# Optimization experiments

Hardware: AMD Instinct MI355X
Metric: run time of the kernel (lower is better)

The kernel has to match this reference:

```python
import jax, jax.numpy as jnp
import numpy as np

B, T, U, C, N, K = 128, 800, 64, 80, 512, 10


def setup_inputs() -> dict:
    key = jax.random.key(0)
    ks = jax.random.split(key, 8)
    s = 0.05
    return {
        "x": jax.random.normal(ks[0], (B, T, 3), jnp.float32),
        "sentence_inputs": jax.random.uniform(ks[1], (B, U, C), jnp.float32),
        "sentence_lengths": jax.random.randint(ks[2], (B,), 1, U + 1, jnp.int32),
        "W_x": jax.random.normal(ks[3], (3 + C, 4 * N), jnp.float32) * s,
        "W_h": jax.random.normal(ks[4], (N, 4 * N), jnp.float32) * s,
        "b": jnp.zeros((4 * N,), jnp.float32),
        "W_win": jax.random.normal(ks[5], (N, 3 * K), jnp.float32) * s,
        "b_win": jnp.zeros((3 * K,), jnp.float32),
    }


def reference(x, sentence_inputs, sentence_lengths, W_x, W_h, b, W_win, b_win):
    # mask over character positions: [B, 1, U]
    u = jnp.arange(1, U + 1, dtype=jnp.float32)                 # 1..U as in tf.range
    mask = (jnp.arange(U)[None, :] < sentence_lengths[:, None]).astype(jnp.float32)

    def step(carry, x_t):
        h, c, kappa, w = carry
        xi = jnp.concatenate([x_t, w], axis=-1)                 # [B, 3+C]
        z = xi @ W_x + h @ W_h + b                              # [B, 4N]
        zi, zf, zg, zo = jnp.split(z, 4, axis=-1)               # keras gate order i,f,c,o
        i = jax.nn.sigmoid(zi)
        f = jax.nn.sigmoid(zf)
        g = jnp.tanh(zg)
        o = jax.nn.sigmoid(zo)
        c = f * c + i * g
        h = o * jnp.tanh(c)
        win = h @ W_win + b_win                                 # [B, 3K]
        a_hat, b_hat, k_hat = jnp.split(win, 3, axis=-1)
        alpha = jnp.exp(a_hat)[:, :, None]                      # [B, K, 1]
        beta = jnp.exp(b_hat)[:, :, None]
        kappa = kappa + jnp.exp(k_hat)                          # [B, K]
        # Gaussian window weights phi: [B, U]
        phi = jnp.sum(alpha * jnp.exp(-beta * (kappa[:, :, None] - u) ** 2), axis=1)
        phi = phi * mask
        w = jnp.einsum('bu,buc->bc', phi, sentence_inputs)      # [B, C]
        return (h, c, kappa, w), (h, phi, w)

    h0 = jnp.zeros((B, N), jnp.float32)
    c0 = jnp.zeros((B, N), jnp.float32)
    k0 = jnp.zeros((B, K), jnp.float32)
    w0 = jnp.zeros((B, C), jnp.float32)
    _, (h_seq, phi_seq, w_seq) = jax.lax.scan(
        step, (h0, c0, k0, w0), jnp.swapaxes(x, 0, 1))
    # time-major -> batch-major
    return (jnp.swapaxes(h_seq, 0, 1),
            jnp.swapaxes(phi_seq, 0, 1),
            jnp.swapaxes(w_seq, 0, 1))
```

## Files before the change

### kernel.cpp

```cpp
#include <hip/hip_runtime.h>
#include <hip/hip_bf16.h>

#define Tt   800
#define Uu   64
#define Cc   80
#define NBLK 128
#define ASTR 648
#define ALIMB 10368

#define HB_G    32768
#define HB_BUF  16384
#define HB_LIMB 8192

#define OUT_PHI 52428800u
#define OUT_W   58982400u

#define WS_HBUF  0u
#define WS_SEQ   524288u
#define WS_SENTT 524800u
#define WS_NEED  3146240u
#define POLL_CAP 2000000

typedef __attribute__((ext_vector_type(4))) int   i32x4;
typedef __attribute__((ext_vector_type(8))) short short8;
typedef __attribute__((ext_vector_type(4))) float f32x4;
typedef unsigned long long u64;

__device__ __forceinline__ float b2f(unsigned short u){ unsigned int i = ((unsigned int)u)<<16; float f; __builtin_memcpy(&f,&i,4); return f; }
__device__ __forceinline__ unsigned short f2b(float f){ __hip_bfloat16 h = __float2bfloat16(f); unsigned short u; __builtin_memcpy(&u,&h,2); return u; }
__device__ __forceinline__ float sigm(float v){ return 1.f/(1.f + __expf(-v)); }
__device__ __forceinline__ float tanh_(float v){ return 1.f - 2.f/(1.f + __expf(2.f*v)); }

__device__ __forceinline__ void drain_vm(){ asm volatile("s_waitcnt vmcnt(0)" ::: "memory"); }
#define WAIT_VM(N) asm volatile("s_waitcnt vmcnt(" #N ")" ::: "memory")

__device__ __forceinline__ void gld16(i32x4* dst, const void* addr) {
  asm volatile("global_load_dwordx4 %0, %1, off sc0 sc1" : "=v"(*dst) : "v"(addr));
}
__device__ __forceinline__ void gst16(void* addr, i32x4 v) {
  asm volatile("global_store_dwordx4 %0, %1, off sc0 sc1" :: "v"(addr), "v"(v) : "memory");
}
__device__ __forceinline__ int gld4(const int* p) {
  int v;
  asm volatile("global_load_dword %0, %1, off sc0 sc1" : "=v"(v) : "v"(p));
  asm volatile("s_waitcnt vmcnt(0)" ::: "memory");
  return v;
}
__device__ __forceinline__ void gst4(int* p, int v) {
  asm volatile("global_store_dword %0, %1, off sc0 sc1" :: "v"(p), "v"(v) : "memory");
}

__global__ void prep(const float* __restrict__ sent,
                     unsigned short* __restrict__ hbuf, int* __restrict__ seq,
                     float* __restrict__ sentT) {
  int i = blockIdx.x*256 + threadIdx.x;
  if (i < 262144) hbuf[i] = 0;
  else if (i < 262272) seq[i - 262144] = 0;
  int j = i - 262272;
  if (j >= 0 && j < 655360) {
    int r = j / 5120, rem = j % 5120, c = rem >> 6, u = rem & 63;
    sentT[j] = sent[r*5120 + u*80 + c];
  }
}

__global__ __launch_bounds__(512, 1) void rnn_main(
    const float* __restrict__ x,
    const int*   __restrict__ slen,
    const float* __restrict__ bias,
    const float* __restrict__ bwin,
    const float* __restrict__ Wwin,
    const float* __restrict__ Wx,
    const float* __restrict__ Wh,
    unsigned short* __restrict__ hbuf,
    int* __restrict__ seq,
    const float* __restrict__ sentT,
    float* __restrict__ out)
{
  __shared__ __align__(16) unsigned short lA[2*ALIMB];
  __shared__ __align__(16) unsigned short lWwF[32768];
  __shared__ __align__(16) float lPart[8*2*64*4];
  __shared__ float lWin[16*32];
  __shared__ float lE[16*32];
  __shared__ float lKap[16*16];
  __shared__ float lPhi[16*64];
  __shared__ __align__(16) unsigned short lHout[2*16*32];
  __shared__ float lBwin[32];
  __shared__ int   lLen[16];

  const int g    = blockIdx.x >> 4;
  const int jj   = blockIdx.x & 15;
  const int grow = g*16 + jj;
  const int tid  = threadIdx.x;
  const int wave = tid >> 6;
  const int lane = tid & 63;
  const int l15  = lane & 15, lhi = lane >> 4;

  int* seqG = seq + g*16;
  unsigned short* hbG = hbuf + g*HB_G;

  for (int i = tid; i < 2*ALIMB/4; i += 512) ((u64*)lA)[i] = 0;
  for (int e = tid; e < 16384; e += 512) {
    int j = e & 7, ln = (e >> 3) & 63, nt = (e >> 9) & 1, kt = e >> 10;
    int k   = kt*32 + (ln >> 4)*8 + j;
    int col = nt*16 + (ln & 15);
    float v = (col < 30) ? Wwin[k*30 + col] : 0.f;
    unsigned short hi = f2b(v);
    lWwF[e]         = hi;
    lWwF[16384 + e] = f2b(v - b2f(hi));
  }
  if (tid < 32)  lBwin[tid] = (tid < 30) ? bwin[tid] : 0.f;
  if (tid < 16)  lLen[tid]  = slen[g*16 + tid];
  for (int i = tid; i < 256; i += 512) lKap[i] = 0.f;

  short8 bfh[20], bfl[20];
  const int zc = (l15 >> 2)*512 + jj*32 + wave*4 + (l15 & 3);
  #pragma unroll
  for (int kt = 0; kt < 20; ++kt) {
    short8 hv, lv;
    #pragma unroll
    for (int j = 0; j < 8; ++j) {
      int k = kt*32 + lhi*8 + j;
      float v;
      if (k < 512)      v = Wh[(size_t)k*2048 + zc];
      else if (k < 515) v = Wx[(size_t)(k-512)*2048 + zc];
      else if (k < 544) v = 0.f;
      else if (k < 624) v = Wx[(size_t)(3 + (k-544))*2048 + zc];
      else              v = 0.f;
      unsigned short hh = f2b(v);
      hv[j] = (short)hh;
      lv[j] = (short)f2b(v - b2f(hh));
    }
    bfh[kt] = hv;
    bfl[kt] = lv;
  }
  const float bias_r = bias[zc];
  __syncthreads();

  float c_reg[4] = {0.f,0.f,0.f,0.f};

  auto phaseW = [&](int tt, bool writeState) {
    {
      f32x4 aw0 = {0.f,0.f,0.f,0.f}, aw1 = {0.f,0.f,0.f,0.f};
      #pragma unroll
      for (int kk = 0; kk < 2; ++kk) {
        const int kt = wave*2 + kk;
        short8 ah = *(const short8*)&lA[l15*ASTR + kt*32 + lhi*8];
        short8 al = *(const short8*)&lA[ALIMB + l15*ASTR + kt*32 + lhi*8];
        short8 bh0 = *(const short8*)&lWwF[((kt*2+0)*64 + lane)*8];
        short8 bl0 = *(const short8*)&lWwF[16384 + ((kt*2+0)*64 + lane)*8];
        short8 bh1 = *(const short8*)&lWwF[((kt*2+1)*64 + lane)*8];
        short8 bl1 = *(const short8*)&lWwF[16384 + ((kt*2+1)*64 + lane)*8];
        aw0 = __builtin_amdgcn_mfma_f32_16x16x32_bf16(ah, bh0, aw0, 0,0,0);
        aw0 = __builtin_amdgcn_mfma_f32_16x16x32_bf16(ah, bl0, aw0, 0,0,0);
        aw0 = __builtin_amdgcn_mfma_f32_16x16x32_bf16(al, bh0, aw0, 0,0,0);
        aw1 = __builtin_amdgcn_mfma_f32_16x16x32_bf16(ah, bh1, aw1, 0,0,0);
        aw1 = __builtin_amdgcn_mfma_f32_16x16x32_bf16(ah, bl1, aw1, 0,0,0);
        aw1 = __builtin_amdgcn_mfma_f32_16x16x32_bf16(al, bh1, aw1, 0,0,0);
      }
      *(f32x4*)&lPart[((wave*2+0)*64 + lane)*4] = aw0;
      *(f32x4*)&lPart[((wave*2+1)*64 + lane)*4] = aw1;
    }
    __syncthreads();
    {
      const int nt = tid >> 8, row = (tid >> 4) & 15, col = tid & 15;
      const int ln = ((row >> 2) << 4) | col, reg = row & 3;
      float s = 0.f;
      #pragma unroll
      for (int w = 0; w < 8; ++w) s += lPart[((w*2 + nt)*64 + ln)*4 + reg];
      lWin[row*32 + nt*16 + col] = s + lBwin[nt*16 + col];
    }
    __syncthreads();
    {
      const int r = tid >> 5, j = tid & 31;
      if (j < 30) lE[r*32 + j] = __expf(lWin[r*32 + j]);
    }
    __syncthreads();
    if (tid < 160) {
      const int r = tid / 10, k = tid % 10;
      lKap[r*16 + k] += lE[r*32 + 20 + k];
    }
    __syncthreads();
    #pragma unroll
    for (int it2 = 0; it2 < 2; ++it2) {
      const int pair = tid + it2*512;
      const int r = pair >> 6, u = pair & 63;
      const float u1 = (float)u + 1.f;
      float phi = 0.f;
      #pragma unroll
      for (int k = 0; k < 10; ++k) {
        float d = lKap[r*16 + k] - u1;
        phi += lE[r*32 + k] * __expf(-lE[r*32 + 10 + k] * d * d);
      }
      if (u >= lLen[r]) phi = 0.f;
      lPhi[r*64 + u] = phi;
      if (r == jj) out[OUT_PHI + ((size_t)grow*Tt + tt)*Uu + u] = phi;
    }
    __syncthreads();
    for (int it2 = 0; it2 < 3; ++it2) {
      const int pair = tid + it2*512;
      if (pair < 1280) {
        const int r = pair / 80, c = pair % 80;
        const float* sp = sentT + ((size_t)(g*16 + r)*80 + c)*64;
        float s = 0.f;
        #pragma unroll 8
        for (int u = 0; u < Uu; ++u) s += lPhi[r*64 + u] * sp[u];
        if (r == jj) out[OUT_W + ((size_t)grow*Tt + tt)*Cc + c] = s;
        if (writeState) {
          unsigned short hi = f2b(s);
          lA[r*ASTR + 544 + c]         = hi;
          lA[ALIMB + r*ASTR + 544 + c] = f2b(s - b2f(hi));
        }
      }
    }
    __syncthreads();
  };

  for (int t = 0; t < Tt; ++t) {
    if (t > 0) {
      if (wave == 0) {
        const int* sp = seqG + (lane & 15);
        int it = 0;
        for (;;) {
          int v = gld4(sp);
          if (__all(v >= t)) break;
          if (++it > POLL_CAP) break;
          __builtin_amdgcn_s_sleep(1);
        }
      }
      __syncthreads();
      const unsigned short* hb = hbG + (t&1)*HB_BUF;
      const int r0 = tid >> 6, q0 = lane;
      i32x4 va, vb, vc, vd;
      gld16(&va, hb + r0*512 + q0*8);
      gld16(&vb, hb + (r0+8)*512 + q0*8);
      gld16(&vc, hb + HB_LIMB + r0*512 + q0*8);
      gld16(&vd, hb + HB_LIMB + (r0+8)*512 + q0*8);
      WAIT_VM(0);
      __builtin_amdgcn_sched_barrier(0);
      *(i32x4*)&lA[r0*ASTR + q0*8]             = va;
      *(i32x4*)&lA[(r0+8)*ASTR + q0*8]         = vb;
      *(i32x4*)&lA[ALIMB + r0*ASTR + q0*8]     = vc;
      *(i32x4*)&lA[ALIMB + (r0+8)*ASTR + q0*8] = vd;
    }
    if (tid < 48) {
      const int row = tid / 3, comp = tid % 3;
      float xv = x[((size_t)(g*16 + row)*Tt + t)*3 + comp];
      unsigned short hh = f2b(xv);
      lA[row*ASTR + 512 + comp]         = hh;
      lA[ALIMB + row*ASTR + 512 + comp] = f2b(xv - b2f(hh));
    }
    __syncthreads();

    if (t > 0) phaseW(t-1, true);

    f32x4 acc0 = {0.f,0.f,0.f,0.f}, acc1 = {0.f,0.f,0.f,0.f};
    const int arow = l15*ASTR + lhi*8;
    #pragma unroll
    for (int kt = 0; kt < 20; ++kt) {
      short8 ah = *(const short8*)&lA[arow + kt*32];
      short8 al = *(const short8*)&lA[ALIMB + arow + kt*32];
      acc0 = __builtin_amdgcn_mfma_f32_16x16x32_bf16(ah, bfh[kt], acc0, 0,0,0);
      acc1 = __builtin_amdgcn_mfma_f32_16x16x32_bf16(ah, bfl[kt], acc1, 0,0,0);
      acc1 = __builtin_amdgcn_mfma_f32_16x16x32_bf16(al, bfh[kt], acc1, 0,0,0);
    }

    #pragma unroll
    for (int r = 0; r < 4; ++r) {
      float v   = acc0[r] + acc1[r] + bias_r;
      float t4  = __shfl_xor(v, 4);
      float t8  = __shfl_xor(v, 8);
      float t12 = __shfl_xor(v, 12);
      float ig = sigm(v), fg = sigm(t4), gg = tanh_(t8), og = sigm(t12);
      float cn = fg*c_reg[r] + ig*gg;
      c_reg[r] = cn;
      float h = og*tanh_(cn);
      if (l15 < 4) {
        const int ui = wave*4 + l15;
        const int rr = lhi*4 + r;
        unsigned short h16 = f2b(h);
        lHout[rr*32 + ui]       = h16;
        lHout[512 + rr*32 + ui] = f2b(h - b2f(h16));
        out[((size_t)(g*16 + rr)*Tt + t)*512 + (jj*32 + ui)] = h;
      }
    }
    __syncthreads();

    {
      unsigned short* hbn = hbG + ((t+1)&1)*HB_BUF;
      if (tid < 128) {
        const int rr = tid >> 3, limb = (tid >> 2) & 1, q = tid & 3;
        i32x4 v = *(const i32x4*)&lHout[limb*512 + rr*32 + q*8];
        gst16(hbn + limb*HB_LIMB + rr*512 + jj*32 + q*8, v);
        drain_vm();
      }
    }
    __syncthreads();
    if (tid == 0) gst4(seqG + jj, t+1);
  }

  if (wave == 0) {
    const int* sp = seqG + (lane & 15);
    int it = 0;
    for (;;) {
      int v = gld4(sp);
      if (__all(v >= Tt)) break;
      if (++it > POLL_CAP) break;
      __builtin_amdgcn_s_sleep(1);
    }
  }
  __syncthreads();
  {
    const unsigned short* hb = hbG + (Tt&1)*HB_BUF;
    const int r0 = tid >> 6, q0 = lane;
    i32x4 va, vb, vc, vd;
    gld16(&va, hb + r0*512 + q0*8);
    gld16(&vb, hb + (r0+8)*512 + q0*8);
    gld16(&vc, hb + HB_LIMB + r0*512 + q0*8);
    gld16(&vd, hb + HB_LIMB + (r0+8)*512 + q0*8);
    WAIT_VM(0);
    __builtin_amdgcn_sched_barrier(0);
    *(i32x4*)&lA[r0*ASTR + q0*8]             = va;
    *(i32x4*)&lA[(r0+8)*ASTR + q0*8]         = vb;
    *(i32x4*)&lA[ALIMB + r0*ASTR + q0*8]     = vc;
    *(i32x4*)&lA[ALIMB + (r0+8)*ASTR + q0*8] = vd;
  }
  __syncthreads();
  phaseW(Tt-1, false);
}

extern "C" void kernel_launch(void* const* d_in, const int* in_sizes, int n_in,
                              void* d_out, int out_size, void* d_ws, size_t ws_size,
                              hipStream_t stream) {
  (void)in_sizes; (void)n_in; (void)out_size;
  if (ws_size < WS_NEED) return;
  const float* x    = (const float*)d_in[0];
  const float* sent = (const float*)d_in[1];
  const int*   sl   = (const int*)d_in[2];
  const float* Wx   = (const float*)d_in[3];
  const float* Wh   = (const float*)d_in[4];
  const float* bias = (const float*)d_in[5];
  const float* Wwin = (const float*)d_in[6];
  const float* bwin = (const float*)d_in[7];

  char* ws = (char*)d_ws;
  unsigned short* hbuf = (unsigned short*)(ws + WS_HBUF);
  int* seq = (int*)(ws + WS_SEQ);
  float* sentT = (float*)(ws + WS_SENTT);
  float* out = (float*)d_out;

  prep<<<3587, 256, 0, stream>>>(sent, hbuf, seq, sentT);
  rnn_main<<<NBLK, 512, 0, stream>>>(x, sl, bias, bwin, Wwin, Wx, Wh,
                                     hbuf, seq, sentT, out);
}
```

Before: 12.71 ms.

## Defer output stores past the sequence flag, fuse window exp steps, vectorize sentence reads

Global stores of h, phi and w are staged in LDS and written after the per-step sequence counter is published. This takes them off the critical path between blocks that wait on each other. The window stage merges bias add, exp and the kappa update into one pass, which removes two block barriers. Other changes: the x load is issued together with the hbuf loads, the sentence dot product reads float4, and register pinning plus a waves-per-EU attribute keep the weight fragments in VGPRs. The cost is extra LDS and some reordering, which may raise register pressure.

```diff
diff --git a/kernel.cpp b/kernel.cpp
--- a/kernel.cpp
+++ b/kernel.cpp
@@ -63,7 +63,8 @@
   }
 }
 
-__global__ __launch_bounds__(512, 1) void rnn_main(
+__global__ __launch_bounds__(512, 1) __attribute__((amdgpu_waves_per_eu(1, 2)))
+void rnn_main(
     const float* __restrict__ x,
     const int*   __restrict__ slen,
     const float* __restrict__ bias,
@@ -79,11 +80,12 @@
   __shared__ __align__(16) unsigned short lA[2*ALIMB];
   __shared__ __align__(16) unsigned short lWwF[32768];
   __shared__ __align__(16) float lPart[8*2*64*4];
-  __shared__ float lWin[16*32];
   __shared__ float lE[16*32];
   __shared__ float lKap[16*16];
   __shared__ float lPhi[16*64];
   __shared__ __align__(16) unsigned short lHout[2*16*32];
+  __shared__ float lHf[16*32];
+  __shared__ float lWst[96];
   __shared__ float lBwin[32];
   __shared__ int   lLen[16];
 
@@ -133,12 +135,17 @@
     bfh[kt] = hv;
     bfl[kt] = lv;
   }
+  #pragma unroll
+  for (int kt = 0; kt < 20; ++kt) {
+    asm volatile("" : "+v"(bfh[kt]));
+    asm volatile("" : "+v"(bfl[kt]));
+  }
   const float bias_r = bias[zc];
   __syncthreads();
 
   float c_reg[4] = {0.f,0.f,0.f,0.f};
 
-  auto phaseW = [&](int tt, bool writeState) {
+  auto phaseW = [&](int tt, bool writeState, bool deferOut) {
     {
       f32x4 aw0 = {0.f,0.f,0.f,0.f}, aw1 = {0.f,0.f,0.f,0.f};
       #pragma unroll
@@ -167,17 +174,10 @@
       float s = 0.f;
       #pragma unroll
       for (int w = 0; w < 8; ++w) s += lPart[((w*2 + nt)*64 + ln)*4 + reg];
-      lWin[row*32 + nt*16 + col] = s + lBwin[nt*16 + col];
-    }
-    __syncthreads();
-    {
-      const int r = tid >> 5, j = tid & 31;
-      if (j < 30) lE[r*32 + j] = __expf(lWin[r*32 + j]);
-    }
-    __syncthreads();
-    if (tid < 160) {
-      const int r = tid / 10, k = tid % 10;
-      lKap[r*16 + k] += lE[r*32 + 20 + k];
+      float e = __expf(s + lBwin[nt*16 + col]);
+      lE[row*32 + nt*16 + col] = e;
+      if (nt == 1 && col >= 4 && col < 14)
+        lKap[row*16 + (col - 4)] += e;
     }
     __syncthreads();
     #pragma unroll
@@ -193,18 +193,26 @@
       }
       if (u >= lLen[r]) phi = 0.f;
       lPhi[r*64 + u] = phi;
-      if (r == jj) out[OUT_PHI + ((size_t)grow*Tt + tt)*Uu + u] = phi;
+      if (!deferOut && r == jj)
+        out[OUT_PHI + ((size_t)grow*Tt + tt)*Uu + u] = phi;
     }
     __syncthreads();
     for (int it2 = 0; it2 < 3; ++it2) {
       const int pair = tid + it2*512;
       if (pair < 1280) {
         const int r = pair / 80, c = pair % 80;
-        const float* sp = sentT + ((size_t)(g*16 + r)*80 + c)*64;
+        const float4* sp4 = (const float4*)(sentT + ((size_t)(g*16 + r)*80 + c)*64);
+        const float* ph = &lPhi[r*64];
         float s = 0.f;
-        #pragma unroll 8
-        for (int u = 0; u < Uu; ++u) s += lPhi[r*64 + u] * sp[u];
-        if (r == jj) out[OUT_W + ((size_t)grow*Tt + tt)*Cc + c] = s;
+        #pragma unroll
+        for (int u4 = 0; u4 < 16; ++u4) {
+          float4 sv = sp4[u4];
+          s += ph[u4*4+0]*sv.x + ph[u4*4+1]*sv.y + ph[u4*4+2]*sv.z + ph[u4*4+3]*sv.w;
+        }
+        if (r == jj) {
+          if (deferOut) lWst[c] = s;
+          else out[OUT_W + ((size_t)grow*Tt + tt)*Cc + c] = s;
+        }
         if (writeState) {
           unsigned short hi = f2b(s);
           lA[r*ASTR + 544 + c]         = hi;
@@ -228,30 +236,39 @@
         }
       }
       __syncthreads();
-      const unsigned short* hb = hbG + (t&1)*HB_BUF;
+    }
+    {
+      i32x4 va, vb, vc, vd;
       const int r0 = tid >> 6, q0 = lane;
-      i32x4 va, vb, vc, vd;
-      gld16(&va, hb + r0*512 + q0*8);
-      gld16(&vb, hb + (r0+8)*512 + q0*8);
-      gld16(&vc, hb + HB_LIMB + r0*512 + q0*8);
-      gld16(&vd, hb + HB_LIMB + (r0+8)*512 + q0*8);
+      if (t > 0) {
+        const unsigned short* hb = hbG + (t&1)*HB_BUF;
+        gld16(&va, hb + r0*512 + q0*8);
+        gld16(&vb, hb + (r0+8)*512 + q0*8);
+        gld16(&vc, hb + HB_LIMB + r0*512 + q0*8);
+        gld16(&vd, hb + HB_LIMB + (r0+8)*512 + q0*8);
+      }
+      float xv = 0.f; int xrow = 0, xcomp = 0;
+      if (tid < 48) {
+        xrow = tid / 3; xcomp = tid % 3;
+        xv = x[((size_t)(g*16 + xrow)*Tt + t)*3 + xcomp];
+      }
       WAIT_VM(0);
       __builtin_amdgcn_sched_barrier(0);
-      *(i32x4*)&lA[r0*ASTR + q0*8]             = va;
-      *(i32x4*)&lA[(r0+8)*ASTR + q0*8]         = vb;
-      *(i32x4*)&lA[ALIMB + r0*ASTR + q0*8]     = vc;
-      *(i32x4*)&lA[ALIMB + (r0+8)*ASTR + q0*8] = vd;
-    }
-    if (tid < 48) {
-      const int row = tid / 3, comp = tid % 3;
-      float xv = x[((size_t)(g*16 + row)*Tt + t)*3 + comp];
-      unsigned short hh = f2b(xv);
-      lA[row*ASTR + 512 + comp]         = hh;
-      lA[ALIMB + row*ASTR + 512 + comp] = f2b(xv - b2f(hh));
-    }
-    __syncthreads();
-
-    if (t > 0) phaseW(t-1, true);
+      if (t > 0) {
+        *(i32x4*)&lA[r0*ASTR + q0*8]             = va;
+        *(i32x4*)&lA[(r0+8)*ASTR + q0*8]         = vb;
+        *(i32x4*)&lA[ALIMB + r0*ASTR + q0*8]     = vc;
+        *(i32x4*)&lA[ALIMB + (r0+8)*ASTR + q0*8] = vd;
+      }
+      if (tid < 48) {
+        unsigned short hh = f2b(xv);
+        lA[xrow*ASTR + 512 + xcomp]         = hh;
+        lA[ALIMB + xrow*ASTR + 512 + xcomp] = f2b(xv - b2f(hh));
+      }
+    }
+    __syncthreads();
+
+    if (t > 0) phaseW(t-1, true, true);
 
     f32x4 acc0 = {0.f,0.f,0.f,0.f}, acc1 = {0.f,0.f,0.f,0.f};
     const int arow = l15*ASTR + lhi*8;
@@ -280,7 +297,7 @@
         unsigned short h16 = f2b(h);
         lHout[rr*32 + ui]       = h16;
         lHout[512 + rr*32 + ui] = f2b(h - b2f(h16));
-        out[((size_t)(g*16 + rr)*Tt + t)*512 + (jj*32 + ui)] = h;
+        lHf[rr*32 + ui]         = h;
       }
     }
     __syncthreads();
@@ -296,6 +313,17 @@
     }
     __syncthreads();
     if (tid == 0) gst4(seqG + jj, t+1);
+
+    {
+      const int rr = tid >> 5, ui = tid & 31;
+      out[((size_t)(g*16 + rr)*Tt + t)*512 + jj*32 + ui] = lHf[rr*32 + ui];
+      if (t > 0) {
+        if (tid < 64)
+          out[OUT_PHI + ((size_t)grow*Tt + (t-1))*Uu + tid] = lPhi[jj*64 + tid];
+        else if (tid >= 64 && tid < 144)
+          out[OUT_W + ((size_t)grow*Tt + (t-1))*Cc + (tid - 64)] = lWst[tid - 64];
+      }
+    }
   }
 
   if (wave == 0) {
@@ -325,7 +353,7 @@
     *(i32x4*)&lA[ALIMB + (r0+8)*ASTR + q0*8] = vd;
   }
   __syncthreads();
-  phaseW(Tt-1, false);
+  phaseW(Tt-1, false, false);
 }
 
 extern "C" void kernel_launch(void* const* d_in, const int* in_sizes, int n_in,
```

After: 13.59 ms. 1.07x slower.
